# Performance work log

Measured on AMD Instinct MI355X. Metric: run time of the kernel, lower is better.

The kernel has to match this reference:

```python
import jax, jax.numpy as jnp
import numpy as np

N = 100000      # nodes
E = 600000      # edges
IN = 128        # in_dim
HID = 32        # hidden_dim per head (layer 1)
HEADS = 4       # num_heads (layer 1)
NEG_SLOPE = 0.2 # PyG GATConv default negative_slope


def setup_inputs() -> dict:
    key = jax.random.key(0)
    ks = jax.random.split(key, 10)
    x = jax.random.normal(ks[0], (N, IN), dtype=jnp.float32)
    edge_index = jax.random.randint(ks[1], (2, E), 0, N, dtype=jnp.int64)
    # layer 1 params: W1 [IN, HEADS*HID], attention vectors [HEADS, HID], bias [HEADS*HID]
    W1 = jax.random.normal(ks[2], (IN, HEADS * HID), dtype=jnp.float32) / np.float32(np.sqrt(IN))
    att_src1 = jax.random.normal(ks[3], (HEADS, HID), dtype=jnp.float32) * 0.1
    att_dst1 = jax.random.normal(ks[4], (HEADS, HID), dtype=jnp.float32) * 0.1
    b1 = jnp.zeros((HEADS * HID,), dtype=jnp.float32)
    # layer 2 params: heads=1, out channels=1, concat=False
    W2 = jax.random.normal(ks[5], (HEADS * HID, 1), dtype=jnp.float32) / np.float32(np.sqrt(HEADS * HID))
    att_src2 = jax.random.normal(ks[6], (1, 1), dtype=jnp.float32) * 0.1
    att_dst2 = jax.random.normal(ks[7], (1, 1), dtype=jnp.float32) * 0.1
    b2 = jnp.zeros((1,), dtype=jnp.float32)
    return {"x": x, "edge_index": edge_index, "W1": W1, "att_src1": att_src1,
            "att_dst1": att_dst1, "b1": b1, "W2": W2, "att_src2": att_src2,
            "att_dst2": att_dst2, "b2": b2}


def gat_layer(x, src, dst, W, a_src, a_dst, b, heads, ch, concat):
    """PyG GATConv (eval mode): edge score + segment softmax + scatter aggregate."""
    n = x.shape[0]
    h = (x @ W).reshape(n, heads, ch)                    # [N,H,C]
    e_src = jnp.einsum('nhc,hc->nh', h, a_src)           # alpha_src per node
    e_dst = jnp.einsum('nhc,hc->nh', h, a_dst)           # alpha_dst per node
    e = jax.nn.leaky_relu(e_src[src] + e_dst[dst], NEG_SLOPE)  # [E,H]
    m = jax.ops.segment_max(e, dst, num_segments=n)      # stable softmax per dst
    p = jnp.exp(e - m[dst])
    denom = jax.ops.segment_sum(p, dst, num_segments=n)
    alpha = p / (denom[dst] + 1e-16)                     # [E,H]
    out = jax.ops.segment_sum(alpha[:, :, None] * h[src], dst, num_segments=n)  # [N,H,C]
    out = out.reshape(n, heads * ch) if concat else out.mean(axis=1)
    return out + b


def reference(x, edge_index, W1, att_src1, att_dst1, b1, W2, att_src2, att_dst2, b2):
    n = x.shape[0]
    loops = jnp.arange(n, dtype=edge_index.dtype)        # PyG add_self_loops=True
    src = jnp.concatenate([edge_index[0], loops])
    dst = jnp.concatenate([edge_index[1], loops])
    h1 = gat_layer(x, src, dst, W1, att_src1, att_dst1, b1, HEADS, HID, True)   # [N, HEADS*HID]
    out = gat_layer(h1, src, dst, W2, att_src2, att_dst2, b2, 1, 1, False)      # [N, 1]
    return out
```

## Files before the change

kernel.cpp:

```cpp
#include <hip/hip_runtime.h>
#include <hip/hip_fp16.h>
#include <math.h>

#define N_NODES 100000
#define E_EDGES 600000
#define IN_DIM  128
#define HID     32
#define HEADS   4
#define NEG     0.2f
#define CAP     32

typedef __attribute__((ext_vector_type(8))) _Float16 f16x8;
typedef __attribute__((ext_vector_type(4))) float f32x4;

__device__ __forceinline__ float lrelu(float v) { return v > 0.f ? v : NEG * v; }

#define SWZ(r, byteoff) ((byteoff) ^ (((r) & 7) << 4))


__global__ __launch_bounds__(128) void wprep_kernel(const float* __restrict__ W1,
                                                    const float* __restrict__ as1,
                                                    const float* __restrict__ ad1,
                                                    __half* __restrict__ wtx,
                                                    int* __restrict__ cnt) {
    int tid = blockIdx.x * 128 + threadIdx.x;
    for (int i = tid; i < N_NODES; i += 144 * 128) cnt[i] = 0;

    int b = blockIdx.x;
    int t = threadIdx.x;
    float v;
    if (b < 128) {
        v = W1[t * 128 + b];
    } else if (b < 136) {
        int h = b - 128;
        int hh = h & 3;
        const float* av = (h < 4) ? (as1 + hh * 32) : (ad1 + hh * 32);
        float s = 0.f;
        #pragma unroll 8
        for (int c = 0; c < 32; ++c) s += W1[t * 128 + hh * 32 + c] * av[c];
        v = s;
    } else {
        v = 0.f;
    }
    wtx[b * 128 + t] = __float2half(v);
}


__global__ __launch_bounds__(256) void gemm1_kernel(const float* __restrict__ x,
                                                    const __half* __restrict__ wtx,
                                                    __half* __restrict__ h1h,
                                                    float* __restrict__ aab) {
    __shared__ __half lx[64 * 128];
    __shared__ __half lw[144 * 128];
    int t = threadIdx.x;
    int row0 = blockIdx.x * 64;

    #pragma unroll
    for (int it = 0; it < 9; ++it) {
        int idx = t + it * 256;
        int r = idx >> 4, c = idx & 15;
        uint4 v = ((const uint4*)wtx)[idx];
        *(uint4*)((char*)lw + SWZ(r, r * 256 + c * 16)) = v;
    }
    #pragma unroll
    for (int it = 0; it < 8; ++it) {
        int idx = t + it * 256;
        int r = idx >> 5, c = idx & 31;
        int gr = row0 + r;
        float4 v = make_float4(0.f, 0.f, 0.f, 0.f);
        if (gr < N_NODES) v = ((const float4*)x)[gr * 32 + c];
        union { uint2 u; __half2 h[2]; } pk;
        pk.h[0] = __floats2half2_rn(v.x, v.y);
        pk.h[1] = __floats2half2_rn(v.z, v.w);
        *(uint2*)((char*)lx + SWZ(r, r * 256 + c * 8)) = pk.u;
    }
    __syncthreads();

    int w = t >> 6, lane = t & 63;
    int li = lane & 15, g = lane >> 4;
    int arow = w * 16 + li;

    f16x8 af[4];
    #pragma unroll
    for (int kt = 0; kt < 4; ++kt)
        af[kt] = *(const f16x8*)((const char*)lx + SWZ(arow, arow * 256 + kt * 64 + g * 16));

    f32x4 acc[9];
    #pragma unroll
    for (int ct = 0; ct < 9; ++ct) acc[ct] = (f32x4){0.f, 0.f, 0.f, 0.f};

    #pragma unroll
    for (int ct = 0; ct < 9; ++ct) {
        int n = ct * 16 + li;
        #pragma unroll
        for (int kt = 0; kt < 4; ++kt) {
            f16x8 bf = *(const f16x8*)((const char*)lw + SWZ(n, n * 256 + kt * 64 + g * 16));
            acc[ct] = __builtin_amdgcn_mfma_f32_16x16x32_f16(af[kt], bf, acc[ct], 0, 0, 0);
        }
    }

    int gr0 = row0 + w * 16 + g * 4;
    #pragma unroll
    for (int ct = 0; ct < 8; ++ct) {
        int col = ct * 16 + li;
        #pragma unroll
        for (int q = 0; q < 4; ++q) {
            int gr = gr0 + q;
            if (gr < N_NODES) h1h[gr * 128 + col] = __float2half(acc[ct][q]);
        }
    }
    if (li < 8) {
        #pragma unroll
        for (int q = 0; q < 4; ++q) {
            int gr = gr0 + q;
            if (gr < N_NODES) aab[gr * 8 + li] = acc[8][q];
        }
    }
}


__global__ __launch_bounds__(256) void scatter_kernel(const int* __restrict__ ei,
                                                      const float* __restrict__ aab,
                                                      int* __restrict__ cnt,
                                                      uint4* __restrict__ edges) {
    int e = blockIdx.x * 256 + threadIdx.x;
    if (e >= E_EDGES) return;
    int s = ei[e];
    int d = ei[E_EDGES + e];
    int slot = atomicAdd(&cnt[d], 1);
    if (slot >= CAP) return;
    float4 asv = *(const float4*)&aab[s * 8];
    float4 adv = *(const float4*)&aab[d * 8 + 4];
    float p0 = __expf(lrelu(asv.x + adv.x));
    float p1 = __expf(lrelu(asv.y + adv.y));
    float p2 = __expf(lrelu(asv.z + adv.z));
    float p3 = __expf(lrelu(asv.w + adv.w));
    union { __half2 h; unsigned u; } a, b;
    a.h = __floats2half2_rn(p0, p1);
    b.h = __floats2half2_rn(p2, p3);
    uint4 rec;
    rec.x = (unsigned)s; rec.y = a.u; rec.z = b.u; rec.w = 0;
    edges[d * CAP + slot] = rec;
}


__global__ __launch_bounds__(256) void agg1_kernel(const __half* __restrict__ h1h,
                                                   const float* __restrict__ aab,
                                                   const int* __restrict__ cnt,
                                                   const uint4* __restrict__ edges,
                                                   const float* __restrict__ b1,
                                                   const float* __restrict__ W2,
                                                   const float* __restrict__ att_src2,
                                                   const float* __restrict__ att_dst2,
                                                   float* __restrict__ h2,
                                                   float* __restrict__ a2s,
                                                   float* __restrict__ a2d) {
    int tid = threadIdx.x;
    int c = tid & 15;
    int n = blockIdx.x * 16 + (tid >> 4);
    int head = c >> 2;
    int deg = min(cnt[n], CAP);
    const uint4* eb = edges + (size_t)n * CAP;

    __half2 acc01 = __half2(0.f, 0.f), acc23 = acc01, acc45 = acc01, acc67 = acc01;
    float den = 0.f;

    for (int e = 0; e < deg; ++e) {
        uint4 rec = eb[e];
        int s = (int)rec.x;
        union { unsigned u; __half2 h; } py;
        py.u = (head & 2) ? rec.z : rec.y;
        __half ph = (head & 1) ? __high2half(py.h) : __low2half(py.h);
        __half2 pp = __half2half2(ph);
        union { uint4 u; __half2 h[4]; } hv;
        hv.u = *(const uint4*)&h1h[s * 128 + c * 8];
        acc01 = __hfma2(pp, hv.h[0], acc01);
        acc23 = __hfma2(pp, hv.h[1], acc23);
        acc45 = __hfma2(pp, hv.h[2], acc45);
        acc67 = __hfma2(pp, hv.h[3], acc67);
        den += __half2float(ph);
    }

    float s0 = __low2float(acc01), s1 = __high2float(acc01);
    float s2 = __low2float(acc23), s3 = __high2float(acc23);
    float s4 = __low2float(acc45), s5 = __high2float(acc45);
    float s6 = __low2float(acc67), s7 = __high2float(acc67);

    {
        float p = __expf(lrelu(aab[n * 8 + head] + aab[n * 8 + 4 + head]));
        union { uint4 u; __half2 h[4]; } hv;
        hv.u = *(const uint4*)&h1h[n * 128 + c * 8];
        float2 f0 = __half22float2(hv.h[0]), f1 = __half22float2(hv.h[1]);
        float2 f2 = __half22float2(hv.h[2]), f3 = __half22float2(hv.h[3]);
        s0 += p * f0.x; s1 += p * f0.y; s2 += p * f1.x; s3 += p * f1.y;
        s4 += p * f2.x; s5 += p * f2.y; s6 += p * f3.x; s7 += p * f3.y;
        den += p;
    }

    float inv = 1.f / (den + 1e-16f);
    float4 bv0 = ((const float4*)b1)[c * 2];
    float4 bv1 = ((const float4*)b1)[c * 2 + 1];
    float o0 = s0 * inv + bv0.x, o1 = s1 * inv + bv0.y;
    float o2 = s2 * inv + bv0.z, o3 = s3 * inv + bv0.w;
    float o4 = s4 * inv + bv1.x, o5 = s5 * inv + bv1.y;
    float o6 = s6 * inv + bv1.z, o7 = s7 * inv + bv1.w;

    float4 wv0 = ((const float4*)W2)[c * 2];
    float4 wv1 = ((const float4*)W2)[c * 2 + 1];
    float pp = o0 * wv0.x + o1 * wv0.y + o2 * wv0.z + o3 * wv0.w
             + o4 * wv1.x + o5 * wv1.y + o6 * wv1.z + o7 * wv1.w;
    #pragma unroll
    for (int m = 1; m <= 8; m <<= 1) pp += __shfl_xor(pp, m, 64);
    if (c == 0) {
        h2[n] = pp;
        a2s[n] = pp * att_src2[0];
        a2d[n] = pp * att_dst2[0];
    }
}


__global__ __launch_bounds__(256) void agg2_kernel(const float* __restrict__ h2,
                                                   const float* __restrict__ a2s,
                                                   const float* __restrict__ a2d,
                                                   const int* __restrict__ cnt,
                                                   const uint4* __restrict__ edges,
                                                   const float* __restrict__ b2,
                                                   float* __restrict__ out) {
    int n = blockIdx.x * 256 + threadIdx.x;
    if (n >= N_NODES) return;
    float adn = a2d[n];
    int deg = min(cnt[n], CAP);
    const uint4* eb = edges + (size_t)n * CAP;
    float num = 0.f, den = 0.f;
    for (int i = 0; i < deg; i += 4) {
        int s[4]; bool val[4]; float as_[4], hs[4];
        #pragma unroll
        for (int j = 0; j < 4; ++j) {
            val[j] = (i + j) < deg;
            s[j] = val[j] ? (int)eb[i + j].x : n;
        }
        #pragma unroll
        for (int j = 0; j < 4; ++j) as_[j] = a2s[s[j]];
        #pragma unroll
        for (int j = 0; j < 4; ++j) hs[j] = h2[s[j]];
        #pragma unroll
        for (int j = 0; j < 4; ++j) {
            float p = val[j] ? __expf(lrelu(as_[j] + adn)) : 0.f;
            num += p * hs[j];
            den += p;
        }
    }
    {
        float p = __expf(lrelu(a2s[n] + adn));
        num += p * h2[n];
        den += p;
    }
    out[n] = num / (den + 1e-16f) + b2[0];
}


extern "C" void kernel_launch(void* const* d_in, const int* in_sizes, int n_in,
                              void* d_out, int out_size, void* d_ws, size_t ws_size,
                              hipStream_t stream) {
    const float* x        = (const float*)d_in[0];
    const int*   ei       = (const int*)d_in[1];
    const float* W1       = (const float*)d_in[2];
    const float* att_src1 = (const float*)d_in[3];
    const float* att_dst1 = (const float*)d_in[4];
    const float* b1       = (const float*)d_in[5];
    const float* W2       = (const float*)d_in[6];
    const float* att_src2 = (const float*)d_in[7];
    const float* att_dst2 = (const float*)d_in[8];
    const float* b2       = (const float*)d_in[9];
    float* out = (float*)d_out;

    char* ws = (char*)d_ws;
    size_t off = 0;
    auto alloc = [&](size_t bytes) {
        char* p = ws + off;
        off = (off + bytes + 255) & ~(size_t)255;
        return p;
    };
    __half* h1h    = (__half*)alloc((size_t)N_NODES * 128 * 2);
    float*  aab    = (float*)alloc((size_t)N_NODES * 8 * 4);
    __half* wtx    = (__half*)alloc((size_t)144 * 128 * 2);
    float*  h2     = (float*)alloc((size_t)N_NODES * 4);
    float*  a2s    = (float*)alloc((size_t)N_NODES * 4);
    float*  a2d    = (float*)alloc((size_t)N_NODES * 4);
    int*    cnt    = (int*)alloc((size_t)N_NODES * 4);
    uint4*  edges  = (uint4*)alloc((size_t)N_NODES * CAP * 16);

    const int NB_NODE = (N_NODES + 255) / 256;
    const int NB_EDGE = (E_EDGES + 255) / 256;
    const int NB_AGG1 = N_NODES / 16;
    const int NB_GEMM = (N_NODES + 63) / 64;

    wprep_kernel<<<144, 128, 0, stream>>>(W1, att_src1, att_dst1, wtx, cnt);
    gemm1_kernel<<<NB_GEMM, 256, 0, stream>>>(x, wtx, h1h, aab);
    scatter_kernel<<<NB_EDGE, 256, 0, stream>>>(ei, aab, cnt, edges);
    agg1_kernel<<<NB_AGG1, 256, 0, stream>>>(h1h, aab, cnt, edges,
                                             b1, W2, att_src2, att_dst2,
                                             h2, a2s, a2d);
    agg2_kernel<<<NB_NODE, 256, 0, stream>>>(h2, a2s, a2d, cnt, edges, b2, out);
}
```

Baseline: 202.1 us.

## Store only source indices in CSR buckets and compute edge scores in aggregation

The scatter kernel now writes only 4-byte source indices per bucket slot instead of 16-byte records holding fp16 exp scores, and it no longer depends on the GEMM output. Edge attention exponentials are recomputed in agg1 from the aab array, with the next neighbor index prefetched each iteration. This shrinks scatter write traffic and the bucket footprint read by agg1 and agg2, at the cost of an extra gather of aab per edge and redundant exp work across the four threads sharing a head. The denominator is now accumulated from the fp32 score rather than the fp16-rounded one. The prefetch reads one slot past the last edge, which is why the buffer gets 64 elements of padding.

```diff
diff --git a/kernel.cpp b/kernel.cpp
--- a/kernel.cpp
+++ b/kernel.cpp
@@ -46,6 +46,18 @@
 }
 
 
+__global__ __launch_bounds__(256) void scatter_kernel(const int* __restrict__ ei,
+                                                      int* __restrict__ cnt,
+                                                      int* __restrict__ idxb) {
+    int e = blockIdx.x * 256 + threadIdx.x;
+    if (e < E_EDGES) {
+        int d = ei[E_EDGES + e];
+        int slot = atomicAdd(&cnt[d], 1);
+        if (slot < CAP) idxb[d * CAP + slot] = ei[e];
+    }
+}
+
+
 __global__ __launch_bounds__(256) void gemm1_kernel(const float* __restrict__ x,
                                                     const __half* __restrict__ wtx,
                                                     __half* __restrict__ h1h,
@@ -119,35 +131,10 @@
 }
 
 
-__global__ __launch_bounds__(256) void scatter_kernel(const int* __restrict__ ei,
-                                                      const float* __restrict__ aab,
-                                                      int* __restrict__ cnt,
-                                                      uint4* __restrict__ edges) {
-    int e = blockIdx.x * 256 + threadIdx.x;
-    if (e >= E_EDGES) return;
-    int s = ei[e];
-    int d = ei[E_EDGES + e];
-    int slot = atomicAdd(&cnt[d], 1);
-    if (slot >= CAP) return;
-    float4 asv = *(const float4*)&aab[s * 8];
-    float4 adv = *(const float4*)&aab[d * 8 + 4];
-    float p0 = __expf(lrelu(asv.x + adv.x));
-    float p1 = __expf(lrelu(asv.y + adv.y));
-    float p2 = __expf(lrelu(asv.z + adv.z));
-    float p3 = __expf(lrelu(asv.w + adv.w));
-    union { __half2 h; unsigned u; } a, b;
-    a.h = __floats2half2_rn(p0, p1);
-    b.h = __floats2half2_rn(p2, p3);
-    uint4 rec;
-    rec.x = (unsigned)s; rec.y = a.u; rec.z = b.u; rec.w = 0;
-    edges[d * CAP + slot] = rec;
-}
-
-
 __global__ __launch_bounds__(256) void agg1_kernel(const __half* __restrict__ h1h,
                                                    const float* __restrict__ aab,
                                                    const int* __restrict__ cnt,
-                                                   const uint4* __restrict__ edges,
+                                                   const int* __restrict__ idxb,
                                                    const float* __restrict__ b1,
                                                    const float* __restrict__ W2,
                                                    const float* __restrict__ att_src2,
@@ -160,25 +147,25 @@
     int n = blockIdx.x * 16 + (tid >> 4);
     int head = c >> 2;
     int deg = min(cnt[n], CAP);
-    const uint4* eb = edges + (size_t)n * CAP;
+    const int* nb = idxb + (size_t)n * CAP;
+    float adn = aab[n * 8 + 4 + head];
 
     __half2 acc01 = __half2(0.f, 0.f), acc23 = acc01, acc45 = acc01, acc67 = acc01;
     float den = 0.f;
 
+    int s = (deg > 0) ? nb[0] : 0;
     for (int e = 0; e < deg; ++e) {
-        uint4 rec = eb[e];
-        int s = (int)rec.x;
-        union { unsigned u; __half2 h; } py;
-        py.u = (head & 2) ? rec.z : rec.y;
-        __half ph = (head & 1) ? __high2half(py.h) : __low2half(py.h);
-        __half2 pp = __half2half2(ph);
+        int s_next = nb[e + 1];
+        float p = __expf(lrelu(aab[s * 8 + head] + adn));
+        __half2 pp = __float2half2_rn(p);
         union { uint4 u; __half2 h[4]; } hv;
         hv.u = *(const uint4*)&h1h[s * 128 + c * 8];
         acc01 = __hfma2(pp, hv.h[0], acc01);
         acc23 = __hfma2(pp, hv.h[1], acc23);
         acc45 = __hfma2(pp, hv.h[2], acc45);
         acc67 = __hfma2(pp, hv.h[3], acc67);
-        den += __half2float(ph);
+        den += p;
+        s = s_next;
     }
 
     float s0 = __low2float(acc01), s1 = __high2float(acc01);
@@ -187,7 +174,7 @@
     float s6 = __low2float(acc67), s7 = __high2float(acc67);
 
     {
-        float p = __expf(lrelu(aab[n * 8 + head] + aab[n * 8 + 4 + head]));
+        float p = __expf(lrelu(aab[n * 8 + head] + adn));
         union { uint4 u; __half2 h[4]; } hv;
         hv.u = *(const uint4*)&h1h[n * 128 + c * 8];
         float2 f0 = __half22float2(hv.h[0]), f1 = __half22float2(hv.h[1]);
@@ -223,21 +210,21 @@
                                                    const float* __restrict__ a2s,
                                                    const float* __restrict__ a2d,
                                                    const int* __restrict__ cnt,
-                                                   const uint4* __restrict__ edges,
+                                                   const int* __restrict__ idxb,
                                                    const float* __restrict__ b2,
                                                    float* __restrict__ out) {
     int n = blockIdx.x * 256 + threadIdx.x;
     if (n >= N_NODES) return;
     float adn = a2d[n];
     int deg = min(cnt[n], CAP);
-    const uint4* eb = edges + (size_t)n * CAP;
+    const int* nb = idxb + (size_t)n * CAP;
     float num = 0.f, den = 0.f;
     for (int i = 0; i < deg; i += 4) {
         int s[4]; bool val[4]; float as_[4], hs[4];
         #pragma unroll
         for (int j = 0; j < 4; ++j) {
             val[j] = (i + j) < deg;
-            s[j] = val[j] ? (int)eb[i + j].x : n;
+            s[j] = val[j] ? nb[i + j] : n;
         }
         #pragma unroll
         for (int j = 0; j < 4; ++j) as_[j] = a2s[s[j]];
@@ -288,7 +275,7 @@
     float*  a2s    = (float*)alloc((size_t)N_NODES * 4);
     float*  a2d    = (float*)alloc((size_t)N_NODES * 4);
     int*    cnt    = (int*)alloc((size_t)N_NODES * 4);
-    uint4*  edges  = (uint4*)alloc((size_t)N_NODES * CAP * 16);
+    int*    idxb   = (int*)alloc(((size_t)N_NODES * CAP + 64) * 4);
 
     const int NB_NODE = (N_NODES + 255) / 256;
     const int NB_EDGE = (E_EDGES + 255) / 256;
@@ -296,10 +283,10 @@
     const int NB_GEMM = (N_NODES + 63) / 64;
 
     wprep_kernel<<<144, 128, 0, stream>>>(W1, att_src1, att_dst1, wtx, cnt);
+    scatter_kernel<<<NB_EDGE, 256, 0, stream>>>(ei, cnt, idxb);
     gemm1_kernel<<<NB_GEMM, 256, 0, stream>>>(x, wtx, h1h, aab);
-    scatter_kernel<<<NB_EDGE, 256, 0, stream>>>(ei, aab, cnt, edges);
-    agg1_kernel<<<NB_AGG1, 256, 0, stream>>>(h1h, aab, cnt, edges,
+    agg1_kernel<<<NB_AGG1, 256, 0, stream>>>(h1h, aab, cnt, idxb,
                                              b1, W2, att_src2, att_dst2,
                                              h2, a2s, a2d);
-    agg2_kernel<<<NB_NODE, 256, 0, stream>>>(h2, a2s, a2d, cnt, edges, b2, out);
-}
+    agg2_kernel<<<NB_NODE, 256, 0, stream>>>(h2, a2s, a2d, cnt, idxb, b2, out);
+}
```

New measurement: 191.8 us. -5.1%, faster.
